# Kernel tuning notes

Hardware: AMD Instinct MI355X
Metric: run time of the kernel (lower is better)

The kernel has to match this reference:

```python
import jax, jax.numpy as jnp
import numpy as np

N, E, D = 50000, 800000, 128
EPS_BN = 1e-5   # torch BatchNorm1d default eps
EPS_AGG = 1e-6  # aggregation denominator eps


def setup_inputs() -> dict:
    key = jax.random.key(0)
    ks = jax.random.split(key, 20)
    s = 1.0 / np.sqrt(D)
    inp = {
        'h': jax.random.normal(ks[0], (N, D), jnp.float32),
        'e': jax.random.normal(ks[1], (E, D), jnp.float32),
    }
    for i, name in enumerate(['A1', 'A2', 'A3', 'B1', 'B2', 'B3']):
        inp['W_' + name] = (jax.random.normal(ks[2 + i], (D, D), jnp.float32) * s)
        inp['b_' + name] = (jax.random.normal(ks[8 + i], (D,), jnp.float32) * s)
    inp['gamma_e'] = jnp.ones((D,), jnp.float32)
    inp['beta_e'] = jnp.zeros((D,), jnp.float32)
    inp['gamma_h'] = jnp.ones((D,), jnp.float32)
    inp['beta_h'] = jnp.zeros((D,), jnp.float32)
    inp['src'] = jax.random.randint(ks[14], (E,), 0, N, dtype=jnp.int32)
    inp['dst'] = jax.random.randint(ks[15], (E,), 0, N, dtype=jnp.int32)
    return inp


def _bn(x, gamma, beta):
    # BatchNorm1d in training mode: biased batch statistics per channel
    mu = jnp.mean(x, axis=0)
    var = jnp.var(x, axis=0)
    return (x - mu) * jax.lax.rsqrt(var + EPS_BN) * gamma + beta


def reference(h, e, W_A1, b_A1, W_A2, b_A2, W_A3, b_A3,
              W_B1, b_B1, W_B2, b_B2, W_B3, b_B3,
              gamma_e, beta_e, gamma_h, beta_h, src, dst):
    n = h.shape[0]
    A1h = h @ W_A1 + b_A1
    A2h = h @ W_A2 + b_A2
    A3h = h @ W_A3 + b_A3
    B1h = h @ W_B1 + b_B1
    B2h = h @ W_B2 + b_B2
    B3e = e @ W_B3 + b_B3

    # Edge gate: e_ji (forward graph) == e_ik (reverse graph) by construction
    e_pre = B1h[src] + B2h[dst] + B3e            # [E, D]
    e_act = jax.nn.relu(_bn(e_pre, gamma_e, beta_e)) + e  # residual
    sigma = jax.nn.sigmoid(e_act)                # [E, D]

    seg = lambda v, idx: jax.ops.segment_sum(v, idx, num_segments=n)
    # forward aggregation at dst, backward aggregation (reverse graph) at src
    h_fwd = seg(sigma * A2h[src], dst) / (seg(sigma, dst) + EPS_AGG)
    h_bwd = seg(sigma * A3h[dst], src) / (seg(sigma, src) + EPS_AGG)

    h_new = A1h + h_fwd + h_bwd
    h_out = jax.nn.relu(_bn(h_new, gamma_h, beta_h)) + h  # residual; dropout p=0
    return h_out
```

## Files before the change

kernel.cpp:

```cpp
#include <hip/hip_runtime.h>
#include <hip/hip_bf16.h>

#define N_NODES 50000
#define N_EDGES 800000
#define D 128
#define NODE_TILES 3125
#define EDGE_TILES 50000

typedef __attribute__((ext_vector_type(4))) float f32x4;
typedef __attribute__((ext_vector_type(2))) float f32x2;
typedef __attribute__((ext_vector_type(8))) short bf16x8;

__device__ __forceinline__ unsigned short f2bf(float f) {
    __hip_bfloat16 h = __float2bfloat16(f);
    return __builtin_bit_cast(unsigned short, h);
}
__device__ __forceinline__ float bf2f(short s) {
    return __builtin_bit_cast(float, ((unsigned)(unsigned short)s) << 16);
}
__device__ __forceinline__ float bflo(unsigned u) { return __builtin_bit_cast(float, u << 16); }
__device__ __forceinline__ float bfhi(unsigned u) { return __builtin_bit_cast(float, u & 0xffff0000u); }

struct WPtrs   { const float* p[6]; };
struct NodeArgs{ const float* bias[3]; unsigned short* out[3]; int widx[3]; };


__global__ __launch_bounds__(256) void k_prep(WPtrs wp, unsigned short* __restrict__ wfrag) {
    int idx = blockIdx.x * 256 + threadIdx.x;
    if (idx >= 6 * 16384) return;
    int w  = idx >> 14;
    int r  = idx & 16383;
    int j  = r & 7;
    int l  = (r >> 3) & 63;
    int kc = r >> 9;
    int ki = kc >> 3, ct = kc & 7;
    int k  = ki * 32 + ((l >> 4) << 3) + j;
    int c  = ct * 16 + (l & 15);
    wfrag[idx] = f2bf(wp.p[w][k * D + c]);
}

__global__ __launch_bounds__(256) void k_node_gemm(const float* __restrict__ x,
                                                   const unsigned short* __restrict__ wfrag,
                                                   NodeArgs na, int ntiles) {
    __shared__ unsigned short ldsw[16384];
    const int z = blockIdx.z;
    {
        const uint4* sp = (const uint4*)(wfrag + (size_t)na.widx[z] * 16384);
        uint4* dp = (uint4*)ldsw;
        for (int i = threadIdx.x; i < 2048; i += 256) dp[i] = sp[i];
    }
    __syncthreads();
    const int lane = threadIdx.x & 63, wave = threadIdx.x >> 6;
    const int tile = blockIdx.x * 4 + wave;
    if (tile >= ntiles) return;
    const int lrow = lane & 15, lgrp = lane >> 4;

    const float* bias = na.bias[z];
    float bias_r[8];
#pragma unroll
    for (int ct = 0; ct < 8; ct++) bias_r[ct] = bias[ct * 16 + lrow];

    f32x4 acc[8];
#pragma unroll
    for (int ct = 0; ct < 8; ct++) acc[ct] = (f32x4)0.0f;

    const float* arow = x + (size_t)(tile * 16 + lrow) * D + lgrp * 8;
#pragma unroll
    for (int ki = 0; ki < 4; ki++) {
        f32x4 a0 = *(const f32x4*)(arow + ki * 32);
        f32x4 a1 = *(const f32x4*)(arow + ki * 32 + 4);
        bf16x8 af;
#pragma unroll
        for (int q = 0; q < 4; q++) { af[q] = (short)f2bf(a0[q]); af[q + 4] = (short)f2bf(a1[q]); }
#pragma unroll
        for (int ct = 0; ct < 8; ct++) {
            bf16x8 bf = *(const bf16x8*)(ldsw + ((ki * 8 + ct) * 64 + lane) * 8);
            acc[ct] = __builtin_amdgcn_mfma_f32_16x16x32_bf16(af, bf, acc[ct], 0, 0, 0);
        }
    }
    unsigned short* out16 = na.out[z];
#pragma unroll
    for (int j = 0; j < 4; j++) {
        bf16x8 pk;
#pragma unroll
        for (int ct = 0; ct < 8; ct++) pk[ct] = (short)f2bf(acc[ct][j] + bias_r[ct]);
        int rr = tile * 16 + lgrp * 4 + j;
        *(bf16x8*)(out16 + (size_t)rr * 128 + lrow * 8) = pk;
    }
}

__global__ __launch_bounds__(256) void k_hist(const int* __restrict__ src, const int* __restrict__ dst,
                                              int* __restrict__ cnt_f, int* __restrict__ cnt_b) {
    int e = blockIdx.x * 256 + threadIdx.x;
    if (e < N_EDGES) {
        atomicAdd(&cnt_f[dst[e]], 1);
        atomicAdd(&cnt_b[src[e]], 1);
    }
}

__global__ __launch_bounds__(1024) void k_scan(const int* __restrict__ cntf, int* __restrict__ offf,
                                               const int* __restrict__ cntb, int* __restrict__ offb) {
    const int* cnt = blockIdx.x ? cntb : cntf;
    int* off = blockIdx.x ? offb : offf;
    const int CH = 49;
    int t = threadIdx.x;
    int base = t * CH;
    int s = 0;
    for (int j = 0; j < CH; j++) { int i = base + j; s += (i < N_NODES) ? cnt[i] : 0; }
    __shared__ int tot[1024];
    tot[t] = s;
    __syncthreads();
    for (int d = 1; d < 1024; d <<= 1) {
        int v = (t >= d) ? tot[t - d] : 0;
        __syncthreads();
        tot[t] += v;
        __syncthreads();
    }
    int run = tot[t] - s;
    for (int j = 0; j < CH; j++) {
        int i = base + j;
        if (i < N_NODES) { run += cnt[i]; off[i + 1] = run; }
    }
    if (t == 0) off[0] = 0;
}

__global__ __launch_bounds__(256) void k_rank(const int* __restrict__ src, const int* __restrict__ dst,
                                              const int* __restrict__ off_f, const int* __restrict__ off_b,
                                              int* __restrict__ cnt2_f, int* __restrict__ cnt2_b,
                                              int2* __restrict__ idx_f, int2* __restrict__ idx_b) {
    int e = blockIdx.x * 256 + threadIdx.x;
    if (e < N_EDGES) {
        int d = dst[e], s = src[e];
        int rf = atomicAdd(&cnt2_f[d], 1);
        idx_f[off_f[d] + rf] = make_int2(e, s);
        int rb = atomicAdd(&cnt2_b[s], 1);
        idx_b[off_b[s] + rb] = make_int2(e, d);
    }
}

__global__ __launch_bounds__(256) void k_stats(
        const unsigned short* __restrict__ epre16,
        const unsigned short* __restrict__ B1p, const unsigned short* __restrict__ B2p,
        const int* __restrict__ src, const int* __restrict__ dst,
        float* __restrict__ ssum, float* __restrict__ sssq) {
    const int lane = threadIdx.x & 63, wave = threadIdx.x >> 6;
    const int t = lane & 15, sub = lane >> 4;
    float ss[8] = {0,0,0,0,0,0,0,0}, sq[8] = {0,0,0,0,0,0,0,0};
    const int NG = N_EDGES / 16;
    for (int q = blockIdx.x * 4 + wave; q < NG; q += gridDim.x * 4) {
        const int rb = q * 16 + sub;
        int s4[4], d4[4];
#pragma unroll
        for (int u = 0; u < 4; u++) { s4[u] = src[rb + u * 4]; d4[u] = dst[rb + u * 4]; }
        bf16x8 p[4], g1[4], g2[4];
#pragma unroll
        for (int u = 0; u < 4; u++) p[u]  = *(const bf16x8*)(epre16 + (((size_t)(rb + u * 4)) << 7) + t * 8);
#pragma unroll
        for (int u = 0; u < 4; u++) g1[u] = *(const bf16x8*)(B1p + (size_t)s4[u] * 128 + t * 8);
#pragma unroll
        for (int u = 0; u < 4; u++) g2[u] = *(const bf16x8*)(B2p + (size_t)d4[u] * 128 + t * 8);
#pragma unroll
        for (int u = 0; u < 4; u++)
#pragma unroll
            for (int ct = 0; ct < 8; ct++) {
                float v = bf2f(p[u][ct]) + bf2f(g1[u][ct]) + bf2f(g2[u][ct]);
                ss[ct] += v; sq[ct] += v * v;
            }
    }
#pragma unroll
    for (int ct = 0; ct < 8; ct++) {
        float a = ss[ct], b = sq[ct];
        a += __shfl_xor(a, 16); a += __shfl_xor(a, 32);
        b += __shfl_xor(b, 16); b += __shfl_xor(b, 32);
        if (lane < 16) {
            atomicAdd(&ssum[ct * 16 + lane], a);
            atomicAdd(&sssq[ct * 16 + lane], b);
        }
    }
}

__global__ void k_bnparam(const float* __restrict__ ssum, const float* __restrict__ sssq,
                          const float* __restrict__ gamma, const float* __restrict__ beta,
                          float cnt, float* __restrict__ scale, float* __restrict__ shift) {
    int c = threadIdx.x;
    float mu  = ssum[c] / cnt;
    float var = sssq[c] / cnt - mu * mu;
    float rs  = rsqrtf(var + 1e-5f);
    float sc  = rs * gamma[c];
    scale[c] = sc;
    shift[c] = beta[c] - mu * sc;
}

__global__ __launch_bounds__(256) void k_sigma(const float* __restrict__ e,
        const unsigned short* __restrict__ epre16,
        const unsigned short* __restrict__ B1p, const unsigned short* __restrict__ B2p,
        const int* __restrict__ src, const int* __restrict__ dst,
        unsigned char* __restrict__ sigma,
        const float* __restrict__ scale_e, const float* __restrict__ shift_e) {
    const int lane = threadIdx.x & 63, wave = threadIdx.x >> 6;
    const int t = lane & 15, sub = lane >> 4;
    float sc[8], sh[8];
#pragma unroll
    for (int ct = 0; ct < 8; ct++) {
        int ch = ct * 16 + t;
        sc[ct] = scale_e[ch]; sh[ct] = shift_e[ch];
    }
    const int NQ = N_EDGES / 4;
    for (int q = blockIdx.x * 4 + wave; q < NQ; q += gridDim.x * 4) {
        const int r = q * 4 + sub;
        const int s = src[r], d = dst[r];
        bf16x8 pk = *(const bf16x8*)(epre16 + (((size_t)r) << 7) + t * 8);
        bf16x8 g1 = *(const bf16x8*)(B1p + (size_t)s * 128 + t * 8);
        bf16x8 g2 = *(const bf16x8*)(B2p + (size_t)d * 128 + t * 8);
        const float* er = e + (size_t)r * 128 + t;
        float sg[8];
#pragma unroll
        for (int ct = 0; ct < 8; ct++) {
            float v  = bf2f(pk[ct]) + bf2f(g1[ct]) + bf2f(g2[ct]);
            float xn = v * sc[ct] + sh[ct];
            float ea = fmaxf(xn, 0.0f) + er[ct * 16];
            sg[ct] = 1.0f / (1.0f + __expf(-ea));
        }
        int lo = 0, hi = 0;
        lo = __builtin_amdgcn_cvt_pk_fp8_f32(sg[0], sg[1], lo, false);
        lo = __builtin_amdgcn_cvt_pk_fp8_f32(sg[2], sg[3], lo, true);
        hi = __builtin_amdgcn_cvt_pk_fp8_f32(sg[4], sg[5], hi, false);
        hi = __builtin_amdgcn_cvt_pk_fp8_f32(sg[6], sg[7], hi, true);
        uint2 v; v.x = (unsigned)lo; v.y = (unsigned)hi;
        *(uint2*)(sigma + (size_t)r * 128 + t * 8) = v;
    }
}

__global__ __launch_bounds__(256) void k_aggregate(
        const unsigned char* __restrict__ sigma,
        const unsigned short* __restrict__ A1p, const unsigned short* __restrict__ A2p,
        const unsigned short* __restrict__ A3p,
        const int* __restrict__ off_f, const int2* __restrict__ idx_f,
        const int* __restrict__ off_b, const int2* __restrict__ idx_b,
        float* __restrict__ hnewp, float* __restrict__ ssum, float* __restrict__ sssq) {
    const int lane = threadIdx.x & 63, wave = threadIdx.x >> 6;
    const int wgl = blockIdx.x * 4 + wave;
    float ps0 = 0, pq0 = 0, ps1 = 0, pq1 = 0;
#pragma unroll 1
    for (int n = wgl * 4; n < wgl * 4 + 4; n++) {
        float fn0 = 0, fd0 = 0, fn1 = 0, fd1 = 0;
        float bn0 = 0, bd0 = 0, bn1 = 0, bd1 = 0;
        {
            int beg = off_f[n], end = off_f[n + 1];
            int i = beg;
            for (; i + 4 <= end; i += 4) {
                int2 e0 = idx_f[i], e1 = idx_f[i + 1], e2 = idx_f[i + 2], e3 = idx_f[i + 3];
                unsigned short w0 = *(const unsigned short*)(sigma + (size_t)e0.x * 128 + 2 * lane);
                unsigned short w1 = *(const unsigned short*)(sigma + (size_t)e1.x * 128 + 2 * lane);
                unsigned short w2 = *(const unsigned short*)(sigma + (size_t)e2.x * 128 + 2 * lane);
                unsigned short w3 = *(const unsigned short*)(sigma + (size_t)e3.x * 128 + 2 * lane);
                unsigned a0 = *(const unsigned*)(A2p + (size_t)e0.y * 128 + 2 * lane);
                unsigned a1 = *(const unsigned*)(A2p + (size_t)e1.y * 128 + 2 * lane);
                unsigned a2 = *(const unsigned*)(A2p + (size_t)e2.y * 128 + 2 * lane);
                unsigned a3 = *(const unsigned*)(A2p + (size_t)e3.y * 128 + 2 * lane);
                f32x2 s0 = __builtin_amdgcn_cvt_pk_f32_fp8((int)w0, false);
                f32x2 s1 = __builtin_amdgcn_cvt_pk_f32_fp8((int)w1, false);
                f32x2 s2 = __builtin_amdgcn_cvt_pk_f32_fp8((int)w2, false);
                f32x2 s3 = __builtin_amdgcn_cvt_pk_f32_fp8((int)w3, false);
                fn0 += s0.x * bflo(a0) + s1.x * bflo(a1) + s2.x * bflo(a2) + s3.x * bflo(a3);
                fd0 += s0.x + s1.x + s2.x + s3.x;
                fn1 += s0.y * bfhi(a0) + s1.y * bfhi(a1) + s2.y * bfhi(a2) + s3.y * bfhi(a3);
                fd1 += s0.y + s1.y + s2.y + s3.y;
            }
            for (; i < end; i++) {
                int2 e0 = idx_f[i];
                unsigned short w0 = *(const unsigned short*)(sigma + (size_t)e0.x * 128 + 2 * lane);
                unsigned a0 = *(const unsigned*)(A2p + (size_t)e0.y * 128 + 2 * lane);
                f32x2 s0 = __builtin_amdgcn_cvt_pk_f32_fp8((int)w0, false);
                fn0 += s0.x * bflo(a0); fd0 += s0.x;
                fn1 += s0.y * bfhi(a0); fd1 += s0.y;
            }
        }
        {
            int beg = off_b[n], end = off_b[n + 1];
            int i = beg;
            for (; i + 4 <= end; i += 4) {
                int2 e0 = idx_b[i], e1 = idx_b[i + 1], e2 = idx_b[i + 2], e3 = idx_b[i + 3];
                unsigned short w0 = *(const unsigned short*)(sigma + (size_t)e0.x * 128 + 2 * lane);
                unsigned short w1 = *(const unsigned short*)(sigma + (size_t)e1.x * 128 + 2 * lane);
                unsigned short w2 = *(const unsigned short*)(sigma + (size_t)e2.x * 128 + 2 * lane);
                unsigned short w3 = *(const unsigned short*)(sigma + (size_t)e3.x * 128 + 2 * lane);
                unsigned a0 = *(const unsigned*)(A3p + (size_t)e0.y * 128 + 2 * lane);
                unsigned a1 = *(const unsigned*)(A3p + (size_t)e1.y * 128 + 2 * lane);
                unsigned a2 = *(const unsigned*)(A3p + (size_t)e2.y * 128 + 2 * lane);
                unsigned a3 = *(const unsigned*)(A3p + (size_t)e3.y * 128 + 2 * lane);
                f32x2 s0 = __builtin_amdgcn_cvt_pk_f32_fp8((int)w0, false);
                f32x2 s1 = __builtin_amdgcn_cvt_pk_f32_fp8((int)w1, false);
                f32x2 s2 = __builtin_amdgcn_cvt_pk_f32_fp8((int)w2, false);
                f32x2 s3 = __builtin_amdgcn_cvt_pk_f32_fp8((int)w3, false);
                bn0 += s0.x * bflo(a0) + s1.x * bflo(a1) + s2.x * bflo(a2) + s3.x * bflo(a3);
                bd0 += s0.x + s1.x + s2.x + s3.x;
                bn1 += s0.y * bfhi(a0) + s1.y * bfhi(a1) + s2.y * bfhi(a2) + s3.y * bfhi(a3);
                bd1 += s0.y + s1.y + s2.y + s3.y;
            }
            for (; i < end; i++) {
                int2 e0 = idx_b[i];
                unsigned short w0 = *(const unsigned short*)(sigma + (size_t)e0.x * 128 + 2 * lane);
                unsigned a0 = *(const unsigned*)(A3p + (size_t)e0.y * 128 + 2 * lane);
                f32x2 s0 = __builtin_amdgcn_cvt_pk_f32_fp8((int)w0, false);
                bn0 += s0.x * bflo(a0); bd0 += s0.x;
                bn1 += s0.y * bfhi(a0); bd1 += s0.y;
            }
        }
        unsigned a1 = *(const unsigned*)(A1p + (size_t)n * 128 + 2 * lane);
        float hv0 = bflo(a1) + fn0 / (fd0 + 1e-6f) + bn0 / (bd0 + 1e-6f);
        float hv1 = bfhi(a1) + fn1 / (fd1 + 1e-6f) + bn1 / (bd1 + 1e-6f);
        f32x2 hv; hv.x = hv0; hv.y = hv1;
        *(f32x2*)(hnewp + (size_t)n * 128 + 2 * lane) = hv;
        ps0 += hv0; pq0 += hv0 * hv0;
        ps1 += hv1; pq1 += hv1 * hv1;
    }
    __shared__ float red[4][64][4];
    red[wave][lane][0] = ps0; red[wave][lane][1] = pq0;
    red[wave][lane][2] = ps1; red[wave][lane][3] = pq1;
    __syncthreads();
    if (threadIdx.x < 64) {
        int l = threadIdx.x;
        float s0 = 0, q0 = 0, s1 = 0, q1 = 0;
#pragma unroll
        for (int w = 0; w < 4; w++) {
            s0 += red[w][l][0]; q0 += red[w][l][1];
            s1 += red[w][l][2]; q1 += red[w][l][3];
        }
        int c0 = (((2 * l) & 7) << 4) + (l >> 2);
        atomicAdd(&ssum[c0], s0);      atomicAdd(&sssq[c0], q0);
        atomicAdd(&ssum[c0 + 16], s1); atomicAdd(&sssq[c0 + 16], q1);
    }
}

__global__ __launch_bounds__(256) void k_hout(const float* __restrict__ hnewp,
        const float* __restrict__ h, const float* __restrict__ scale,
        const float* __restrict__ shift, float* __restrict__ out) {
    __shared__ float sc[128], sh[128];
    if (threadIdx.x < 128) { sc[threadIdx.x] = scale[threadIdx.x]; sh[threadIdx.x] = shift[threadIdx.x]; }
    __syncthreads();
    const int total = N_NODES * 32;
    for (int i = blockIdx.x * blockDim.x + threadIdx.x; i < total; i += gridDim.x * blockDim.x) {
        int r = i >> 5, c4 = (i & 31) * 4;
        f32x4 hh = *(const f32x4*)(h + (size_t)r * 128 + c4);
        f32x4 o;
#pragma unroll
        for (int k = 0; k < 4; k++) {
            int ch = c4 + k;
            int p = (ch >> 4) + ((ch & 15) << 3);
            float v = hnewp[(size_t)r * 128 + p];
            o[k] = fmaxf(v * sc[ch] + sh[ch], 0.0f) + hh[k];
        }
        *(f32x4*)(out + (size_t)r * 128 + c4) = o;
    }
}

extern "C" void kernel_launch(void* const* d_in, const int* in_sizes, int n_in,
                              void* d_out, int out_size, void* d_ws, size_t ws_size,
                              hipStream_t stream) {
    const float* h = (const float*)d_in[0];
    const float* e = (const float*)d_in[1];
    const float* W[6] = {(const float*)d_in[2], (const float*)d_in[4], (const float*)d_in[6],
                         (const float*)d_in[8], (const float*)d_in[10], (const float*)d_in[12]};
    const float* b[6] = {(const float*)d_in[3], (const float*)d_in[5], (const float*)d_in[7],
                         (const float*)d_in[9], (const float*)d_in[11], (const float*)d_in[13]};
    const float* gamma_e = (const float*)d_in[14];
    const float* beta_e  = (const float*)d_in[15];
    const float* gamma_h = (const float*)d_in[16];
    const float* beta_h  = (const float*)d_in[17];
    const int* src = (const int*)d_in[18];
    const int* dst = (const int*)d_in[19];
    float* out = (float*)d_out;

    char* ws = (char*)d_ws;
    unsigned short* wfrag = (unsigned short*)(ws);
    float* scale_e = (float*)(ws + 196608);
    float* shift_e = (float*)(ws + 197120);
    float* scale_h = (float*)(ws + 197632);
    float* shift_h = (float*)(ws + 198144);
    float* ssum_e  = (float*)(ws + 198656);
    float* sssq_e  = (float*)(ws + 199168);
    float* ssum_h  = (float*)(ws + 199680);
    float* sssq_h  = (float*)(ws + 200192);
    int*   cnt_f   = (int*)(ws + 200704);
    int*   cnt_b   = (int*)(ws + 400704);
    int*   cnt2_f  = (int*)(ws + 600704);
    int*   cnt2_b  = (int*)(ws + 800704);
    int*   off_f   = (int*)(ws + 1000704);
    int*   off_b   = (int*)(ws + 1200768);
    unsigned short* slot0 = (unsigned short*)(ws + 1400832);
    unsigned short* slot1 = slot0 + 6400000;
    unsigned short* slot2 = slot1 + 6400000;
    unsigned char* sigma = (unsigned char*)(ws + 39800832);
    int2*  idx_f   = (int2*)(ws + 142200832);
    int2*  idx_b   = idx_f + N_EDGES;
    float* hnewp   = (float*)(ws + 155000832);
    unsigned short* epre16 = (unsigned short*)(ws + 180600832);

    hipMemsetAsync(ws + 198656, 0, 802048, stream);

    WPtrs wp;
    for (int i = 0; i < 6; i++) wp.p[i] = W[i];
    k_prep<<<384, 256, 0, stream>>>(wp, wfrag);

    NodeArgs nb;
    nb.bias[0] = b[3]; nb.bias[1] = b[4]; nb.bias[2] = b[4];
    nb.out[0] = slot0; nb.out[1] = slot1; nb.out[2] = slot1;
    nb.widx[0] = 3;    nb.widx[1] = 4;    nb.widx[2] = 4;
    k_node_gemm<<<dim3(782, 1, 2), 256, 0, stream>>>(h, wfrag, nb, NODE_TILES);

    k_hist<<<3125, 256, 0, stream>>>(src, dst, cnt_f, cnt_b);
    k_scan<<<2, 1024, 0, stream>>>(cnt_f, off_f, cnt_b, off_b);
    k_rank<<<3125, 256, 0, stream>>>(src, dst, off_f, off_b, cnt2_f, cnt2_b, idx_f, idx_b);

    NodeArgs ne;
    ne.bias[0] = b[5]; ne.bias[1] = b[5]; ne.bias[2] = b[5];
    ne.out[0] = epre16; ne.out[1] = epre16; ne.out[2] = epre16;
    ne.widx[0] = 5;    ne.widx[1] = 5;    ne.widx[2] = 5;
    k_node_gemm<<<dim3(12500, 1, 1), 256, 0, stream>>>(e, wfrag, ne, EDGE_TILES);

    k_stats<<<2048, 256, 0, stream>>>(epre16, slot0, slot1, src, dst, ssum_e, sssq_e);
    k_bnparam<<<1, 128, 0, stream>>>(ssum_e, sssq_e, gamma_e, beta_e, (float)N_EDGES, scale_e, shift_e);
    k_sigma<<<2048, 256, 0, stream>>>(e, epre16, slot0, slot1, src, dst, sigma, scale_e, shift_e);

    NodeArgs na;
    na.bias[0] = b[0]; na.bias[1] = b[1]; na.bias[2] = b[2];
    na.out[0] = slot0; na.out[1] = slot1; na.out[2] = slot2;
    na.widx[0] = 0;    na.widx[1] = 1;    na.widx[2] = 2;
    k_node_gemm<<<dim3(782, 1, 3), 256, 0, stream>>>(h, wfrag, na, NODE_TILES);

    k_aggregate<<<3125, 256, 0, stream>>>(sigma, slot0, slot1, slot2,
                                          off_f, idx_f, off_b, idx_b, hnewp, ssum_h, sssq_h);
    k_bnparam<<<1, 128, 0, stream>>>(ssum_h, sssq_h, gamma_h, beta_h, (float)N_NODES, scale_h, shift_h);
    k_hout<<<1024, 256, 0, stream>>>(hnewp, h, scale_h, shift_h, out);
}
```

Measured before the change: 1.007 ms.

## Scatter sigma into CSR order for forward and backward aggregation; cache pre-BN sum

The stats kernel now writes the summed pre-BN edge values as bf16, so the sigma kernel no longer re-gathers the B1/B2 rows by src/dst. The sigma kernel scatters each edge's fp8 sigma row into two copies laid out in dst-sorted and src-sorted CSR order. The aggregation kernel can then read sigma contiguously instead of gathering it by edge id, and its index arrays shrink from int2 to int. The cost is an extra bf16 edge-sized write and read, a doubled sigma write done as scattered stores, and per-edge rank arrays.

```diff
diff --git a/kernel.cpp b/kernel.cpp
--- a/kernel.cpp
+++ b/kernel.cpp
@@ -127,21 +127,25 @@
 __global__ __launch_bounds__(256) void k_rank(const int* __restrict__ src, const int* __restrict__ dst,
                                               const int* __restrict__ off_f, const int* __restrict__ off_b,
                                               int* __restrict__ cnt2_f, int* __restrict__ cnt2_b,
-                                              int2* __restrict__ idx_f, int2* __restrict__ idx_b) {
+                                              int* __restrict__ idxn_f, int* __restrict__ idxn_b,
+                                              int* __restrict__ rkf, int* __restrict__ rkb) {
     int e = blockIdx.x * 256 + threadIdx.x;
     if (e < N_EDGES) {
         int d = dst[e], s = src[e];
-        int rf = atomicAdd(&cnt2_f[d], 1);
-        idx_f[off_f[d] + rf] = make_int2(e, s);
-        int rb = atomicAdd(&cnt2_b[s], 1);
-        idx_b[off_b[s] + rb] = make_int2(e, d);
-    }
-}
-
-__global__ __launch_bounds__(256) void k_stats(
+        int sf = off_f[d] + atomicAdd(&cnt2_f[d], 1);
+        idxn_f[sf] = s;
+        rkf[e] = sf;
+        int sb = off_b[s] + atomicAdd(&cnt2_b[s], 1);
+        idxn_b[sb] = d;
+        rkb[e] = sb;
+    }
+}
+
+__global__ __launch_bounds__(256) void k_gather_v(
         const unsigned short* __restrict__ epre16,
         const unsigned short* __restrict__ B1p, const unsigned short* __restrict__ B2p,
         const int* __restrict__ src, const int* __restrict__ dst,
+        unsigned short* __restrict__ vsum16,
         float* __restrict__ ssum, float* __restrict__ sssq) {
     const int lane = threadIdx.x & 63, wave = threadIdx.x >> 6;
     const int t = lane & 15, sub = lane >> 4;
@@ -160,12 +164,16 @@
 #pragma unroll
         for (int u = 0; u < 4; u++) g2[u] = *(const bf16x8*)(B2p + (size_t)d4[u] * 128 + t * 8);
 #pragma unroll
-        for (int u = 0; u < 4; u++)
+        for (int u = 0; u < 4; u++) {
+            bf16x8 o;
 #pragma unroll
             for (int ct = 0; ct < 8; ct++) {
                 float v = bf2f(p[u][ct]) + bf2f(g1[u][ct]) + bf2f(g2[u][ct]);
+                o[ct] = (short)f2bf(v);
                 ss[ct] += v; sq[ct] += v * v;
             }
+            *(bf16x8*)(vsum16 + (((size_t)(rb + u * 4)) << 7) + t * 8) = o;
+        }
     }
 #pragma unroll
     for (int ct = 0; ct < 8; ct++) {
@@ -192,10 +200,9 @@
 }
 
 __global__ __launch_bounds__(256) void k_sigma(const float* __restrict__ e,
-        const unsigned short* __restrict__ epre16,
-        const unsigned short* __restrict__ B1p, const unsigned short* __restrict__ B2p,
-        const int* __restrict__ src, const int* __restrict__ dst,
-        unsigned char* __restrict__ sigma,
+        const unsigned short* __restrict__ vsum16,
+        const int* __restrict__ rkf, const int* __restrict__ rkb,
+        unsigned char* __restrict__ sigf, unsigned char* __restrict__ sigb,
         const float* __restrict__ scale_e, const float* __restrict__ shift_e) {
     const int lane = threadIdx.x & 63, wave = threadIdx.x >> 6;
     const int t = lane & 15, sub = lane >> 4;
@@ -208,16 +215,13 @@
     const int NQ = N_EDGES / 4;
     for (int q = blockIdx.x * 4 + wave; q < NQ; q += gridDim.x * 4) {
         const int r = q * 4 + sub;
-        const int s = src[r], d = dst[r];
-        bf16x8 pk = *(const bf16x8*)(epre16 + (((size_t)r) << 7) + t * 8);
-        bf16x8 g1 = *(const bf16x8*)(B1p + (size_t)s * 128 + t * 8);
-        bf16x8 g2 = *(const bf16x8*)(B2p + (size_t)d * 128 + t * 8);
+        const int sf = rkf[r], sb = rkb[r];
+        bf16x8 pk = *(const bf16x8*)(vsum16 + (((size_t)r) << 7) + t * 8);
         const float* er = e + (size_t)r * 128 + t;
         float sg[8];
 #pragma unroll
         for (int ct = 0; ct < 8; ct++) {
-            float v  = bf2f(pk[ct]) + bf2f(g1[ct]) + bf2f(g2[ct]);
-            float xn = v * sc[ct] + sh[ct];
+            float xn = bf2f(pk[ct]) * sc[ct] + sh[ct];
             float ea = fmaxf(xn, 0.0f) + er[ct * 16];
             sg[ct] = 1.0f / (1.0f + __expf(-ea));
         }
@@ -227,16 +231,17 @@
         hi = __builtin_amdgcn_cvt_pk_fp8_f32(sg[4], sg[5], hi, false);
         hi = __builtin_amdgcn_cvt_pk_fp8_f32(sg[6], sg[7], hi, true);
         uint2 v; v.x = (unsigned)lo; v.y = (unsigned)hi;
-        *(uint2*)(sigma + (size_t)r * 128 + t * 8) = v;
+        *(uint2*)(sigf + (size_t)sf * 128 + t * 8) = v;
+        *(uint2*)(sigb + (size_t)sb * 128 + t * 8) = v;
     }
 }
 
 __global__ __launch_bounds__(256) void k_aggregate(
-        const unsigned char* __restrict__ sigma,
+        const unsigned char* __restrict__ sigf, const unsigned char* __restrict__ sigb,
         const unsigned short* __restrict__ A1p, const unsigned short* __restrict__ A2p,
         const unsigned short* __restrict__ A3p,
-        const int* __restrict__ off_f, const int2* __restrict__ idx_f,
-        const int* __restrict__ off_b, const int2* __restrict__ idx_b,
+        const int* __restrict__ off_f, const int* __restrict__ idxn_f,
+        const int* __restrict__ off_b, const int* __restrict__ idxn_b,
         float* __restrict__ hnewp, float* __restrict__ ssum, float* __restrict__ sssq) {
     const int lane = threadIdx.x & 63, wave = threadIdx.x >> 6;
     const int wgl = blockIdx.x * 4 + wave;
@@ -249,15 +254,15 @@
             int beg = off_f[n], end = off_f[n + 1];
             int i = beg;
             for (; i + 4 <= end; i += 4) {
-                int2 e0 = idx_f[i], e1 = idx_f[i + 1], e2 = idx_f[i + 2], e3 = idx_f[i + 3];
-                unsigned short w0 = *(const unsigned short*)(sigma + (size_t)e0.x * 128 + 2 * lane);
-                unsigned short w1 = *(const unsigned short*)(sigma + (size_t)e1.x * 128 + 2 * lane);
-                unsigned short w2 = *(const unsigned short*)(sigma + (size_t)e2.x * 128 + 2 * lane);
-                unsigned short w3 = *(const unsigned short*)(sigma + (size_t)e3.x * 128 + 2 * lane);
-                unsigned a0 = *(const unsigned*)(A2p + (size_t)e0.y * 128 + 2 * lane);
-                unsigned a1 = *(const unsigned*)(A2p + (size_t)e1.y * 128 + 2 * lane);
-                unsigned a2 = *(const unsigned*)(A2p + (size_t)e2.y * 128 + 2 * lane);
-                unsigned a3 = *(const unsigned*)(A2p + (size_t)e3.y * 128 + 2 * lane);
+                int y0 = idxn_f[i], y1 = idxn_f[i + 1], y2 = idxn_f[i + 2], y3 = idxn_f[i + 3];
+                unsigned short w0 = *(const unsigned short*)(sigf + (size_t)i * 128 + 2 * lane);
+                unsigned short w1 = *(const unsigned short*)(sigf + (size_t)(i + 1) * 128 + 2 * lane);
+                unsigned short w2 = *(const unsigned short*)(sigf + (size_t)(i + 2) * 128 + 2 * lane);
+                unsigned short w3 = *(const unsigned short*)(sigf + (size_t)(i + 3) * 128 + 2 * lane);
+                unsigned a0 = *(const unsigned*)(A2p + (size_t)y0 * 128 + 2 * lane);
+                unsigned a1 = *(const unsigned*)(A2p + (size_t)y1 * 128 + 2 * lane);
+                unsigned a2 = *(const unsigned*)(A2p + (size_t)y2 * 128 + 2 * lane);
+                unsigned a3 = *(const unsigned*)(A2p + (size_t)y3 * 128 + 2 * lane);
                 f32x2 s0 = __builtin_amdgcn_cvt_pk_f32_fp8((int)w0, false);
                 f32x2 s1 = __builtin_amdgcn_cvt_pk_f32_fp8((int)w1, false);
                 f32x2 s2 = __builtin_amdgcn_cvt_pk_f32_fp8((int)w2, false);
@@ -268,9 +273,9 @@
                 fd1 += s0.y + s1.y + s2.y + s3.y;
             }
             for (; i < end; i++) {
-                int2 e0 = idx_f[i];
-                unsigned short w0 = *(const unsigned short*)(sigma + (size_t)e0.x * 128 + 2 * lane);
-                unsigned a0 = *(const unsigned*)(A2p + (size_t)e0.y * 128 + 2 * lane);
+                int y0 = idxn_f[i];
+                unsigned short w0 = *(const unsigned short*)(sigf + (size_t)i * 128 + 2 * lane);
+                unsigned a0 = *(const unsigned*)(A2p + (size_t)y0 * 128 + 2 * lane);
                 f32x2 s0 = __builtin_amdgcn_cvt_pk_f32_fp8((int)w0, false);
                 fn0 += s0.x * bflo(a0); fd0 += s0.x;
                 fn1 += s0.y * bfhi(a0); fd1 += s0.y;
@@ -280,15 +285,15 @@
             int beg = off_b[n], end = off_b[n + 1];
             int i = beg;
             for (; i + 4 <= end; i += 4) {
-                int2 e0 = idx_b[i], e1 = idx_b[i + 1], e2 = idx_b[i + 2], e3 = idx_b[i + 3];
-                unsigned short w0 = *(const unsigned short*)(sigma + (size_t)e0.x * 128 + 2 * lane);
-                unsigned short w1 = *(const unsigned short*)(sigma + (size_t)e1.x * 128 + 2 * lane);
-                unsigned short w2 = *(const unsigned short*)(sigma + (size_t)e2.x * 128 + 2 * lane);
-                unsigned short w3 = *(const unsigned short*)(sigma + (size_t)e3.x * 128 + 2 * lane);
-                unsigned a0 = *(const unsigned*)(A3p + (size_t)e0.y * 128 + 2 * lane);
-                unsigned a1 = *(const unsigned*)(A3p + (size_t)e1.y * 128 + 2 * lane);
-                unsigned a2 = *(const unsigned*)(A3p + (size_t)e2.y * 128 + 2 * lane);
-                unsigned a3 = *(const unsigned*)(A3p + (size_t)e3.y * 128 + 2 * lane);
+                int y0 = idxn_b[i], y1 = idxn_b[i + 1], y2 = idxn_b[i + 2], y3 = idxn_b[i + 3];
+                unsigned short w0 = *(const unsigned short*)(sigb + (size_t)i * 128 + 2 * lane);
+                unsigned short w1 = *(const unsigned short*)(sigb + (size_t)(i + 1) * 128 + 2 * lane);
+                unsigned short w2 = *(const unsigned short*)(sigb + (size_t)(i + 2) * 128 + 2 * lane);
+                unsigned short w3 = *(const unsigned short*)(sigb + (size_t)(i + 3) * 128 + 2 * lane);
+                unsigned a0 = *(const unsigned*)(A3p + (size_t)y0 * 128 + 2 * lane);
+                unsigned a1 = *(const unsigned*)(A3p + (size_t)y1 * 128 + 2 * lane);
+                unsigned a2 = *(const unsigned*)(A3p + (size_t)y2 * 128 + 2 * lane);
+                unsigned a3 = *(const unsigned*)(A3p + (size_t)y3 * 128 + 2 * lane);
                 f32x2 s0 = __builtin_amdgcn_cvt_pk_f32_fp8((int)w0, false);
                 f32x2 s1 = __builtin_amdgcn_cvt_pk_f32_fp8((int)w1, false);
                 f32x2 s2 = __builtin_amdgcn_cvt_pk_f32_fp8((int)w2, false);
@@ -299,9 +304,9 @@
                 bd1 += s0.y + s1.y + s2.y + s3.y;
             }
             for (; i < end; i++) {
-                int2 e0 = idx_b[i];
-                unsigned short w0 = *(const unsigned short*)(sigma + (size_t)e0.x * 128 + 2 * lane);
-                unsigned a0 = *(const unsigned*)(A3p + (size_t)e0.y * 128 + 2 * lane);
+                int y0 = idxn_b[i];
+                unsigned short w0 = *(const unsigned short*)(sigb + (size_t)i * 128 + 2 * lane);
+                unsigned a0 = *(const unsigned*)(A3p + (size_t)y0 * 128 + 2 * lane);
                 f32x2 s0 = __builtin_amdgcn_cvt_pk_f32_fp8((int)w0, false);
                 bn0 += s0.x * bflo(a0); bd0 += s0.x;
                 bn1 += s0.y * bfhi(a0); bd1 += s0.y;
@@ -391,11 +396,15 @@
     unsigned short* slot0 = (unsigned short*)(ws + 1400832);
     unsigned short* slot1 = slot0 + 6400000;
     unsigned short* slot2 = slot1 + 6400000;
-    unsigned char* sigma = (unsigned char*)(ws + 39800832);
-    int2*  idx_f   = (int2*)(ws + 142200832);
-    int2*  idx_b   = idx_f + N_EDGES;
+    unsigned char* sigf = (unsigned char*)(ws + 39800832);
+    int*   idxn_f  = (int*)(ws + 142200832);
+    int*   idxn_b  = (int*)(ws + 145400832);
+    int*   rkf     = (int*)(ws + 148600832);
+    int*   rkb     = (int*)(ws + 151800832);
     float* hnewp   = (float*)(ws + 155000832);
     unsigned short* epre16 = (unsigned short*)(ws + 180600832);
+    unsigned short* vsum16 = (unsigned short*)(ws + 385400832);
+    unsigned char* sigb = (unsigned char*)(ws + 590200832);
 
     hipMemsetAsync(ws + 198656, 0, 802048, stream);
 
@@ -411,7 +420,8 @@
 
     k_hist<<<3125, 256, 0, stream>>>(src, dst, cnt_f, cnt_b);
     k_scan<<<2, 1024, 0, stream>>>(cnt_f, off_f, cnt_b, off_b);
-    k_rank<<<3125, 256, 0, stream>>>(src, dst, off_f, off_b, cnt2_f, cnt2_b, idx_f, idx_b);
+    k_rank<<<3125, 256, 0, stream>>>(src, dst, off_f, off_b, cnt2_f, cnt2_b,
+                                     idxn_f, idxn_b, rkf, rkb);
 
     NodeArgs ne;
     ne.bias[0] = b[5]; ne.bias[1] = b[5]; ne.bias[2] = b[5];
@@ -419,9 +429,9 @@
     ne.widx[0] = 5;    ne.widx[1] = 5;    ne.widx[2] = 5;
     k_node_gemm<<<dim3(12500, 1, 1), 256, 0, stream>>>(e, wfrag, ne, EDGE_TILES);
 
-    k_stats<<<2048, 256, 0, stream>>>(epre16, slot0, slot1, src, dst, ssum_e, sssq_e);
+    k_gather_v<<<2048, 256, 0, stream>>>(epre16, slot0, slot1, src, dst, vsum16, ssum_e, sssq_e);
     k_bnparam<<<1, 128, 0, stream>>>(ssum_e, sssq_e, gamma_e, beta_e, (float)N_EDGES, scale_e, shift_e);
-    k_sigma<<<2048, 256, 0, stream>>>(e, epre16, slot0, slot1, src, dst, sigma, scale_e, shift_e);
+    k_sigma<<<2048, 256, 0, stream>>>(e, vsum16, rkf, rkb, sigf, sigb, scale_e, shift_e);
 
     NodeArgs na;
     na.bias[0] = b[0]; na.bias[1] = b[1]; na.bias[2] = b[2];
@@ -429,8 +439,8 @@
     na.widx[0] = 0;    na.widx[1] = 1;    na.widx[2] = 2;
     k_node_gemm<<<dim3(782, 1, 3), 256, 0, stream>>>(h, wfrag, na, NODE_TILES);
 
-    k_aggregate<<<3125, 256, 0, stream>>>(sigma, slot0, slot1, slot2,
-                                          off_f, idx_f, off_b, idx_b, hnewp, ssum_h, sssq_h);
+    k_aggregate<<<3125, 256, 0, stream>>>(sigf, sigb, slot0, slot1, slot2,
+                                          off_f, idxn_f, off_b, idxn_b, hnewp, ssum_h, sssq_h);
     k_bnparam<<<1, 128, 0, stream>>>(ssum_h, sssq_h, gamma_h, beta_h, (float)N_NODES, scale_h, shift_h);
     k_hout<<<1024, 256, 0, stream>>>(hnewp, h, scale_h, shift_h, out);
 }
```

After: 1.057 ms. +5.0%, slower.
